# Performance work log

Measured on AMD Instinct MI355X. Metric: run time of the kernel, lower is better.

The kernel has to match this reference:

```python
import jax, jax.numpy as jnp
import numpy as np

FILTER_K = 10      # per-class top-K support retention
TAU = 1.0          # temperature
SCALE = 20.0       # prototype logit scale
EPS = 1e-12


def _normalize(x, axis=-1):
    n = jnp.linalg.norm(x, axis=axis, keepdims=True)
    return x / jnp.maximum(n, EPS)


def _entropy(logits):
    p = jax.nn.softmax(logits, axis=1)
    return -(p * jax.nn.log_softmax(logits, axis=1)).sum(axis=1)


def _quantile(x, q):
    # linear-interpolation quantile (matches torch.quantile default)
    s = jnp.sort(x)
    n = x.shape[0]
    pos = q * (n - 1)
    lo = jnp.floor(pos).astype(jnp.int32)
    hi = jnp.minimum(lo + 1, n - 1)
    frac = pos - lo.astype(x.dtype)
    return s[lo] * (1.0 - frac) + s[hi] * frac


def setup_inputs() -> dict:
    key = jax.random.key(0)
    k1, k2, k3, k4, k5 = jax.random.split(key, 5)
    B, D, C = 65536, 512, 50
    feat = jax.random.normal(k1, (B, D), jnp.float32)
    logits_raw = jax.random.normal(k2, (B, C), jnp.float32)
    logits_aug = jax.random.normal(k3, (B, C), jnp.float32)
    W = jax.random.normal(k4, (C, D), jnp.float32) * 0.05  # classifier weight
    b = jax.random.normal(k5, (C,), jnp.float32) * 0.05    # classifier bias
    return {"feat": feat, "logits_raw": logits_raw, "logits_aug": logits_aug, "W": W, "b": b}


def reference(feat, logits_raw, logits_aug, W, b):
    C, D = W.shape
    # --- warmup memory initialized from classifier weights (as in __init__) ---
    wl = W @ W.T + b                       # (C, C)
    p0 = jax.nn.softmax(wl, axis=1)
    lab0 = jnp.argmax(wl, axis=1)          # (C,)
    ent0 = _entropy(wl)
    conf0 = p0.max(axis=1)

    # --- online batch stats ---
    logits = feat @ W.T + b                # (B, C)
    p = jax.nn.softmax(logits, axis=1)
    yhat = jnp.argmax(logits, axis=1)
    ent = _entropy(logits)
    pmax = p.max(axis=1)

    # dynamic entropy-quantile threshold (ent_thresh=None path)
    m = ent.mean()
    dyn_q = jnp.where(m >= 0.45, 0.25, jnp.where(m >= 0.38, 0.3, 0.4))
    thr = _quantile(ent, dyn_q)
    mask = ent <= thr
    # dual-view consistency gate
    mask &= jnp.argmax(logits_raw, axis=1) == jnp.argmax(logits_aug, axis=1)
    # confidence gate
    conf_thr = jnp.where(m >= 0.45, 0.72, 0.62)
    mask &= pmax >= conf_thr

    # --- grown support memory (warmup + accepted batch samples), static shape + valid mask ---
    supports = jnp.concatenate([W, feat], axis=0)          # (C+B, D)
    lab_idx = jnp.concatenate([lab0, yhat], axis=0)        # (C+B,)
    ents = jnp.concatenate([ent0, ent], axis=0)
    conf = jnp.concatenate([conf0, pmax], axis=0)
    valid = jnp.concatenate([jnp.ones((C,), bool), mask], axis=0)

    # --- per-class top-K lowest-entropy pruning (vectorized over classes) ---
    cls_mask = (lab_idx[None, :] == jnp.arange(C)[:, None]) & valid[None, :]  # (C, C+B)
    masked_ent = jnp.where(cls_mask, ents[None, :], jnp.inf)
    order = jnp.argsort(masked_ent, axis=1)
    ranks = jnp.argsort(order, axis=1)                     # rank of each entry within its class
    keep = (cls_mask & (ranks < FILTER_K)).any(axis=0)     # (C+B,)

    # --- confidence-weighted centroids + cosine-sim classification ---
    S = _normalize(supports)
    onehot = jax.nn.one_hot(lab_idx, C, dtype=supports.dtype)
    lab_w = onehot * jnp.maximum(conf, 1e-6)[:, None] * keep[:, None].astype(supports.dtype)
    denom = jnp.maximum(lab_w.sum(axis=0, keepdims=True), EPS)
    centroids = _normalize((lab_w / denom).T @ S)          # (C, D)
    sim = _normalize(feat) @ centroids.T                   # (B, C)
    return SCALE * sim / max(TAU, 1e-6)
```

## Files before the change

### kernel.cpp

```cpp
#include <hip/hip_runtime.h>
#include <math.h>

constexpr int BN = 65536;
constexpr int DK = 512;
constexpr int CN = 50;
constexpr int FILTK = 10;
constexpr int MB = 128;
constexpr int NKS = DK / 32;
constexpr int SELB = 64;
constexpr int CAP = 6144;

typedef __attribute__((ext_vector_type(8))) short short8;
typedef __attribute__((ext_vector_type(4))) float f4;

constexpr int W_SC     = 0;
constexpr int W_H1     = 64;
constexpr int W_H2LO   = 2112;
constexpr int W_H2HI   = 4160;
constexpr int W_H3LO   = 6208;
constexpr int W_H3HI   = 7232;
constexpr int ZERO_WORDS = 8256;
constexpr int W_WFH    = 8256;
constexpr int W_WFL    = W_WFH + 16384;
constexpr int W_CFH    = W_WFL + 16384;
constexpr int W_CFL    = W_CFH + 16384;
constexpr int W_ENT    = W_CFL + 16384;
constexpr int W_PMAX   = W_ENT  + BN;
constexpr int W_YHAT   = W_PMAX + BN;
constexpr int W_CONS   = W_YHAT + BN;
constexpr int W_NORM   = W_CONS + BN;
constexpr int W_LAB0   = W_NORM + BN;
constexpr int W_ENT0   = W_LAB0 + 64;
constexpr int W_CONF0  = W_ENT0 + 64;
constexpr int W_WNORM  = W_CONF0 + 64;
constexpr int LE_CAP   = BN + 64;
constexpr int W_LECLS  = W_WNORM + 64;
constexpr int W_LEENT  = W_LECLS  + LE_CAP;
constexpr int W_LECONF = W_LEENT  + LE_CAP;
constexpr int W_LEORD  = W_LECONF + LE_CAP;
constexpr int W_LESRC  = W_LEORD  + LE_CAP;

struct Scalars {
    float    sum_ent;
    float    mean;
    float    conf_thr;
    float    frac;
    int      klo;
    int      khi;
    unsigned prefix_lo;
    unsigned rank_lo;
    unsigned prefix_hi;
    unsigned rank_hi;
    float    thr;
    unsigned cnt;
    unsigned done1, done2, done3;
};

__device__ __forceinline__ unsigned fkey(float f) {
    unsigned u = __float_as_uint(f);
    return (u & 0x80000000u) ? ~u : (u | 0x80000000u);
}
__device__ __forceinline__ float funkey(unsigned u) {
    return (u & 0x80000000u) ? __uint_as_float(u & 0x7fffffffu) : __uint_as_float(~u);
}

__device__ __forceinline__ short bf16h(float x) {
    unsigned u = __float_as_uint(x);
    return (short)((u + 0x7fffu + ((u >> 16) & 1u)) >> 16);
}
__device__ __forceinline__ float bf16tof(short h) {
    return __uint_as_float(((unsigned)(unsigned short)h) << 16);
}
__device__ __forceinline__ void cvt8(const float* a, short8& h, short8& l) {
    #pragma unroll
    for (int j = 0; j < 8; j++) {
        short hh = bf16h(a[j]);
        h[j] = hh;
        l[j] = bf16h(a[j] - bf16tof(hh));
    }
}
__device__ __forceinline__ int fragidx(int ks, int n, int q, int j) {
    return ks * 2048 + (n >> 4) * 512 + ((n & 15) + 16 * q) * 8 + j;
}

__global__ void init_kernel(const float* __restrict__ W, const float* __restrict__ bias,
                            int* __restrict__ lab0, float* __restrict__ ent0,
                            float* __restrict__ conf0, float* __restrict__ wnorm,
                            unsigned* __restrict__ wsz,
                            short* __restrict__ wfh, short* __restrict__ wfl) {
    const int b = blockIdx.x, l = threadIdx.x;
    if (b >= 64) {
        for (int i = (b - 64) * 64 + l; i < ZERO_WORDS; i += 128) wsz[i] = 0u;
        return;
    }
    {
        int ks = l >> 2, q = l & 3;
        int dst = fragidx(ks, b, q, 0);
        if (b < CN) {
            const float* wp = W + b * DK + l * 8;
            f4 x = *(const f4*)wp, y = *(const f4*)(wp + 4);
            float a8[8] = {x[0], x[1], x[2], x[3], y[0], y[1], y[2], y[3]};
            short8 h, lo2; cvt8(a8, h, lo2);
            *(short8*)(wfh + dst) = h;
            *(short8*)(wfl + dst) = lo2;
        } else {
            short8 z; 
            #pragma unroll
            for (int j = 0; j < 8; j++) z[j] = 0;
            *(short8*)(wfh + dst) = z;
            *(short8*)(wfl + dst) = z;
        }
    }
    if (b >= CN) return;

    __shared__ float wrow[DK];
    const int i = b;
    f4 v0 = *(const f4*)(W + i * DK + l * 4);
    f4 v1 = *(const f4*)(W + i * DK + 256 + l * 4);
    *(f4*)(wrow + l * 4) = v0;
    *(f4*)(wrow + 256 + l * 4) = v1;
    float sq = v0[0]*v0[0] + v0[1]*v0[1] + v0[2]*v0[2] + v0[3]*v0[3]
             + v1[0]*v1[0] + v1[1]*v1[1] + v1[2]*v1[2] + v1[3]*v1[3];
    #pragma unroll
    for (int m = 1; m < 64; m <<= 1) sq += __shfl_xor(sq, m);
    if (l == 0) wnorm[i] = sqrtf(sq);
    __syncthreads();

    float dot = -INFINITY;
    int   ai  = 0x7fffffff;
    if (l < CN) {
        const float* wj = W + l * DK;
        float d2 = 0.f;
        for (int d = 0; d < DK; d += 4) {
            f4 a = *(const f4*)(wrow + d);
            f4 b4 = *(const f4*)(wj + d);
            d2 = fmaf(a[0], b4[0], fmaf(a[1], b4[1], fmaf(a[2], b4[2], fmaf(a[3], b4[3], d2))));
        }
        dot = d2 + bias[l];
        ai  = l;
    }
    float mx = dot; int am = ai;
    #pragma unroll
    for (int m = 32; m >= 1; m >>= 1) {
        float o = __shfl_xor(mx, m); int oi = __shfl_xor(am, m);
        if (o > mx || (o == mx && oi < am)) { mx = o; am = oi; }
    }
    float e = 0.f, te = 0.f;
    if (l < CN) { e = expf(dot - mx); te = e * (dot - mx); }
    #pragma unroll
    for (int m = 1; m < 64; m <<= 1) { e += __shfl_xor(e, m); te += __shfl_xor(te, m); }
    if (l == 0) {
        lab0[i]  = am;
        ent0[i]  = logf(e) - te / e;
        conf0[i] = 1.f / e;
    }
}

template <int MODE>
__global__ __launch_bounds__(256) void gemm_kernel(
        const float* __restrict__ feat,
        const short* __restrict__ bfh, const short* __restrict__ bfl,
        const float* __restrict__ bias,
        float* __restrict__ ent, float* __restrict__ pmaxA,
        int* __restrict__ yhat, float* __restrict__ rnorm,
        const float* __restrict__ lraw, const float* __restrict__ laug,
        unsigned* __restrict__ consp, Scalars* sc, float* __restrict__ outp) {
    constexpr int LSZ = (MODE == 0) ? MB * 65 : 4;
    __shared__ float L[LSZ];
    const int t = threadIdx.x;
    const int w = t >> 6, lane = t & 63, m = lane & 15, q = lane >> 4;
    const int rb = blockIdx.x * MB + w * 32;

    f4 acc[2][4];
    #pragma unroll
    for (int mt = 0; mt < 2; mt++)
        #pragma unroll
        for (int nt = 0; nt < 4; nt++) acc[mt][nt] = (f4){0.f, 0.f, 0.f, 0.f};
    float sq[2] = {0.f, 0.f};

    for (int ks = 0; ks < NKS; ks++) {
        short8 ah[2], al[2];
        #pragma unroll
        for (int mt = 0; mt < 2; mt++) {
            const float* ap = feat + (size_t)(rb + mt * 16 + m) * DK + ks * 32 + q * 8;
            f4 x = *(const f4*)ap;
            f4 y = *(const f4*)(ap + 4);
            float a8[8] = {x[0], x[1], x[2], x[3], y[0], y[1], y[2], y[3]};
            if (MODE == 0) {
                sq[mt] += x[0]*x[0] + x[1]*x[1] + x[2]*x[2] + x[3]*x[3]
                        + y[0]*y[0] + y[1]*y[1] + y[2]*y[2] + y[3]*y[3];
            }
            cvt8(a8, ah[mt], al[mt]);
        }
        short8 bh[4], bl[4];
        #pragma unroll
        for (int nt = 0; nt < 4; nt++) {
            int off = ks * 2048 + nt * 512 + lane * 8;
            bh[nt] = *(const short8*)(bfh + off);
            bl[nt] = *(const short8*)(bfl + off);
        }
        #pragma unroll
        for (int mt = 0; mt < 2; mt++)
            #pragma unroll
            for (int nt = 0; nt < 4; nt++) {
                acc[mt][nt] = __builtin_amdgcn_mfma_f32_16x16x32_bf16(ah[mt], bh[nt], acc[mt][nt], 0, 0, 0);
                acc[mt][nt] = __builtin_amdgcn_mfma_f32_16x16x32_bf16(al[mt], bh[nt], acc[mt][nt], 0, 0, 0);
                acc[mt][nt] = __builtin_amdgcn_mfma_f32_16x16x32_bf16(ah[mt], bl[nt], acc[mt][nt], 0, 0, 0);
            }
    }

    if (MODE == 0) {
        #pragma unroll
        for (int mt = 0; mt < 2; mt++) {
            float s = sq[mt];
            s += __shfl_xor(s, 16);
            s += __shfl_xor(s, 32);
            if (q == 0) rnorm[rb + mt * 16 + m] = sqrtf(s);
        }
        float bc[4];
        #pragma unroll
        for (int nt = 0; nt < 4; nt++) { int c = nt * 16 + m; bc[nt] = (c < CN) ? bias[c] : 0.f; }
        #pragma unroll
        for (int mt = 0; mt < 2; mt++)
            #pragma unroll
            for (int nt = 0; nt < 4; nt++)
                #pragma unroll
                for (int r = 0; r < 4; r++) {
                    int row = w * 32 + mt * 16 + q * 4 + r;
                    L[row * 65 + nt * 16 + m] = acc[mt][nt][r] + bc[nt];
                }
        __syncthreads();
        if (t < MB) {
            int grow = blockIdx.x * MB + t;
            const float* Lr = L + t * 65;
            float mx = Lr[0]; int am = 0;
            #pragma unroll 10
            for (int j = 1; j < CN; j++) { float v = Lr[j]; if (v > mx) { mx = v; am = j; } }
            float s = 0.f, tt = 0.f;
            for (int j = 0; j < CN; j++) {
                float d = Lr[j] - mx;
                float e = expf(d);
                s += e; tt += e * d;
            }
            float ev = logf(s) - tt / s;
            ent  [grow] = ev;
            pmaxA[grow] = 1.f / s;
            yhat [grow] = am;
            const float* rp  = lraw + (size_t)grow * CN;
            const float* apg = laug + (size_t)grow * CN;
            float m1 = rp[0];  int a1 = 0;
            float m2 = apg[0]; int a2 = 0;
            #pragma unroll 10
            for (int j = 1; j < CN; j++) {
                float v1 = rp[j];  if (v1 > m1) { m1 = v1; a1 = j; }
                float v2 = apg[j]; if (v2 > m2) { m2 = v2; a2 = j; }
            }
            consp[grow] = (a1 == a2) ? 1u : 0u;
            float es = ev;
            #pragma unroll
            for (int mk = 1; mk < 64; mk <<= 1) es += __shfl_xor(es, mk);
            if ((t & 63) == 0) atomicAdd(&sc->sum_ent, es);
        }
    } else {
        #pragma unroll
        for (int mt = 0; mt < 2; mt++)
            #pragma unroll
            for (int r = 0; r < 4; r++) {
                int grow = rb + mt * 16 + q * 4 + r;
                float s = 20.f / fmaxf(rnorm[grow], 1e-12f);
                #pragma unroll
                for (int nt = 0; nt < 4; nt++) {
                    int c = nt * 16 + m;
                    if (c < CN) outp[(size_t)grow * CN + c] = acc[mt][nt][r] * s;
                }
            }
    }
}

__global__ __launch_bounds__(256) void sel1_kernel(const float* __restrict__ ent,
                                                   unsigned* __restrict__ H1, Scalars* sc) {
    __shared__ unsigned h[2048];
    __shared__ unsigned part[256];
    __shared__ int last;
    const int t = threadIdx.x;
    for (int b = t; b < 2048; b += 256) h[b] = 0u;
    __syncthreads();
    const int lo = blockIdx.x * (BN / SELB), hi = lo + (BN / SELB);
    for (int i = lo + t; i < hi; i += 256)
        atomicAdd(&h[fkey(ent[i]) >> 21], 1u);
    __syncthreads();
    for (int b = t; b < 2048; b += 256) if (h[b]) atomicAdd(&H1[b], h[b]);
    __threadfence();
    if (t == 0) last = (atomicAdd(&sc->done1, 1u) == SELB - 1) ? 1 : 0;
    __syncthreads();
    if (!last) return;

    for (int b = t; b < 2048; b += 256) h[b] = atomicAdd(&H1[b], 0u);
    __syncthreads();
    unsigned ps = 0;
    #pragma unroll
    for (int j = 0; j < 8; j++) ps += h[t * 8 + j];
    part[t] = ps;
    __syncthreads();
    if (t == 0) {
        float m = sc->sum_ent / (float)BN;
        sc->mean = m;
        float q = (m >= 0.45f) ? 0.25f : ((m >= 0.38f) ? 0.30f : 0.40f);
        sc->conf_thr = (m >= 0.45f) ? 0.72f : 0.62f;
        float pos = q * (float)(BN - 1);
        float flo = floorf(pos);
        sc->frac = pos - flo;
        int klo = (int)flo;
        int khi = klo + 1; if (khi > BN - 1) khi = BN - 1;
        sc->klo = klo; sc->khi = khi;
        for (int pass = 0; pass < 2; pass++) {
            unsigned k = (pass == 0) ? (unsigned)klo : (unsigned)khi;
            unsigned cum = 0; int c = 0;
            for (; c < 255; c++) { unsigned pc = part[c]; if (cum + pc > k) break; cum += pc; }
            int b = c * 8;
            for (; b < c * 8 + 7; b++) { unsigned hb = h[b]; if (cum + hb > k) break; cum += hb; }
            if (pass == 0) { sc->prefix_lo = (unsigned)b; sc->rank_lo = k - cum; }
            else           { sc->prefix_hi = (unsigned)b; sc->rank_hi = k - cum; }
        }
    }
}

__global__ __launch_bounds__(256) void sel2_kernel(const float* __restrict__ ent,
                                                   unsigned* __restrict__ HLO, unsigned* __restrict__ HHI,
                                                   Scalars* sc) {
    __shared__ unsigned hlo[2048], hhi[2048];
    __shared__ unsigned plo_s[256], phi_s[256];
    __shared__ int last;
    const int t = threadIdx.x;
    const unsigned plo = sc->prefix_lo, phi = sc->prefix_hi;
    for (int b = t; b < 2048; b += 256) { hlo[b] = 0u; hhi[b] = 0u; }
    __syncthreads();
    const int lo = blockIdx.x * (BN / SELB), hi = lo + (BN / SELB);
    for (int i = lo + t; i < hi; i += 256) {
        unsigned u = fkey(ent[i]);
        unsigned d1 = u >> 21, d2 = (u >> 10) & 2047u;
        if (d1 == plo) atomicAdd(&hlo[d2], 1u);
        if (d1 == phi) atomicAdd(&hhi[d2], 1u);
    }
    __syncthreads();
    for (int b = t; b < 2048; b += 256) {
        if (hlo[b]) atomicAdd(&HLO[b], hlo[b]);
        if (hhi[b]) atomicAdd(&HHI[b], hhi[b]);
    }
    __threadfence();
    if (t == 0) last = (atomicAdd(&sc->done2, 1u) == SELB - 1) ? 1 : 0;
    __syncthreads();
    if (!last) return;

    for (int b = t; b < 2048; b += 256) { hlo[b] = atomicAdd(&HLO[b], 0u); hhi[b] = atomicAdd(&HHI[b], 0u); }
    __syncthreads();
    unsigned pl = 0, ph = 0;
    #pragma unroll
    for (int j = 0; j < 8; j++) { pl += hlo[t * 8 + j]; ph += hhi[t * 8 + j]; }
    plo_s[t] = pl; phi_s[t] = ph;
    __syncthreads();
    if (t == 0) {
        {
            unsigned k = sc->rank_lo, cum = 0; int c = 0;
            for (; c < 255; c++) { unsigned pc = plo_s[c]; if (cum + pc > k) break; cum += pc; }
            int b = c * 8;
            for (; b < c * 8 + 7; b++) { unsigned hb = hlo[b]; if (cum + hb > k) break; cum += hb; }
            sc->prefix_lo = (plo << 11) | (unsigned)b; sc->rank_lo = k - cum;
        }
        {
            unsigned k = sc->rank_hi, cum = 0; int c = 0;
            for (; c < 255; c++) { unsigned pc = phi_s[c]; if (cum + pc > k) break; cum += pc; }
            int b = c * 8;
            for (; b < c * 8 + 7; b++) { unsigned hb = hhi[b]; if (cum + hb > k) break; cum += hb; }
            sc->prefix_hi = (phi << 11) | (unsigned)b; sc->rank_hi = k - cum;
        }
    }
}

__global__ __launch_bounds__(256) void sel3_kernel(const float* __restrict__ ent,
                                                   unsigned* __restrict__ HLO, unsigned* __restrict__ HHI,
                                                   Scalars* sc) {
    __shared__ unsigned hlo[1024], hhi[1024];
    __shared__ unsigned plo_s[256], phi_s[256];
    __shared__ int last;
    const int t = threadIdx.x;
    const unsigned plo = sc->prefix_lo, phi = sc->prefix_hi;
    for (int b = t; b < 1024; b += 256) { hlo[b] = 0u; hhi[b] = 0u; }
    __syncthreads();
    const int lo = blockIdx.x * (BN / SELB), hi = lo + (BN / SELB);
    for (int i = lo + t; i < hi; i += 256) {
        unsigned u = fkey(ent[i]);
        unsigned p22 = u >> 10, d3 = u & 1023u;
        if (p22 == plo) atomicAdd(&hlo[d3], 1u);
        if (p22 == phi) atomicAdd(&hhi[d3], 1u);
    }
    __syncthreads();
    for (int b = t; b < 1024; b += 256) {
        if (hlo[b]) atomicAdd(&HLO[b], hlo[b]);
        if (hhi[b]) atomicAdd(&HHI[b], hhi[b]);
    }
    __threadfence();
    if (t == 0) last = (atomicAdd(&sc->done3, 1u) == SELB - 1) ? 1 : 0;
    __syncthreads();
    if (!last) return;

    for (int b = t; b < 1024; b += 256) { hlo[b] = atomicAdd(&HLO[b], 0u); hhi[b] = atomicAdd(&HHI[b], 0u); }
    __syncthreads();
    unsigned pl = 0, ph = 0;
    #pragma unroll
    for (int j = 0; j < 4; j++) { pl += hlo[t * 4 + j]; ph += hhi[t * 4 + j]; }
    plo_s[t] = pl; phi_s[t] = ph;
    __syncthreads();
    if (t == 0) {
        float vlo, vhi;
        {
            unsigned k = sc->rank_lo, cum = 0; int c = 0;
            for (; c < 255; c++) { unsigned pc = plo_s[c]; if (cum + pc > k) break; cum += pc; }
            int b = c * 4;
            for (; b < c * 4 + 3; b++) { unsigned hb = hlo[b]; if (cum + hb > k) break; cum += hb; }
            vlo = funkey((plo << 10) | (unsigned)b);
        }
        {
            unsigned k = sc->rank_hi, cum = 0; int c = 0;
            for (; c < 255; c++) { unsigned pc = phi_s[c]; if (cum + pc > k) break; cum += pc; }
            int b = c * 4;
            for (; b < c * 4 + 3; b++) { unsigned hb = hhi[b]; if (cum + hb > k) break; cum += hb; }
            vhi = funkey((phi << 10) | (unsigned)b);
        }
        sc->thr = vlo * (1.f - sc->frac) + vhi * sc->frac;
    }
}

__global__ __launch_bounds__(256) void compact_kernel(
        const float* __restrict__ ent, const float* __restrict__ pmaxA,
        const int* __restrict__ yhat, const unsigned* __restrict__ cons,
        const int* __restrict__ lab0, const float* __restrict__ ent0,
        const float* __restrict__ conf0, Scalars* sc,
        int* le_cls, float* le_ent, float* le_conf, int* le_ord, int* le_src) {
    int i = blockIdx.x * blockDim.x + threadIdx.x;
    if (i < CN) {
        le_cls[i] = lab0[i]; le_ent[i] = ent0[i]; le_conf[i] = conf0[i];
        le_ord[i] = i; le_src[i] = i;
    }
    if (i >= BN) return;
    bool m = (ent[i] <= sc->thr) && (cons[i] != 0u) && (pmaxA[i] >= sc->conf_thr);
    if (m) {
        int pos = (int)atomicAdd(&sc->cnt, 1u);
        int e = CN + pos;
        le_cls[e] = yhat[i]; le_ent[e] = ent[i]; le_conf[e] = pmaxA[i];
        le_ord[e] = CN + i;  le_src[e] = i;
    }
}

__global__ __launch_bounds__(256) void tail2_kernel(
        const Scalars* sc, const int* __restrict__ le_cls,
        const float* __restrict__ le_ent, const float* __restrict__ le_conf,
        const int* __restrict__ le_ord, const int* __restrict__ le_src,
        const float* __restrict__ W, const float* __restrict__ feat,
        const float* __restrict__ wnorm, const float* __restrict__ rnorm,
        short* __restrict__ cfh, short* __restrict__ cfl) {
    const int c = blockIdx.x, t = threadIdx.x;
    if (c >= CN) {
        for (int idx = t; idx < 512; idx += 256) {
            int ks = idx >> 5, rem = idx & 31, qq = rem >> 3, jj = rem & 7;
            int dst = fragidx(ks, c, qq, jj);
            cfh[dst] = 0; cfl[dst] = 0;
        }
        return;
    }
    __shared__ float sent[CAP];
    __shared__ int   sord[CAP];
    __shared__ float sconf[CAP];
    __shared__ int   ssrc[CAP];
    __shared__ float wk[CAP];
    __shared__ float accv[DK];
    __shared__ float red[4];
    __shared__ int   mc_s;
    if (t == 0) mc_s = 0;
    for (int d = t; d < DK; d += 256) accv[d] = 0.f;
    __syncthreads();
    const int M = CN + (int)sc->cnt;
    for (int e = t; e < M; e += 256) {
        if (le_cls[e] == c) {
            int i = atomicAdd(&mc_s, 1);
            if (i < CAP) { sent[i] = le_ent[e]; sord[i] = le_ord[e]; sconf[i] = le_conf[e]; ssrc[i] = le_src[e]; }
        }
    }
    __syncthreads();
    int mc = min(mc_s, CAP);
    for (int i = t; i < mc; i += 256) {
        float v = sent[i]; int o = sord[i]; int r = 0;
        for (int j = 0; j < mc && r < FILTK; j++)
            if (sent[j] < v || (sent[j] == v && sord[j] < o)) r++;
        wk[i] = (r < FILTK) ? fmaxf(sconf[i], 1e-6f) : 0.f;
    }
    __syncthreads();
    for (int i = 0; i < mc; i++) {
        float wgt = wk[i];
        if (wgt <= 0.f) continue;
        int src = ssrc[i];
        bool warm = sord[i] < CN;
        const float* rowp = warm ? (W + src * DK) : (feat + (size_t)src * DK);
        float nr = warm ? wnorm[src] : rnorm[src];
        float k = wgt / fmaxf(nr, 1e-12f);
        for (int d = t; d < DK; d += 256) accv[d] += k * rowp[d];
    }
    __syncthreads();
    float s = 0.f;
    for (int d = t; d < DK; d += 256) { float v = accv[d]; s = fmaf(v, v, s); }
    #pragma unroll
    for (int mk = 1; mk < 64; mk <<= 1) s += __shfl_xor(s, mk);
    if ((t & 63) == 0) red[t >> 6] = s;
    __syncthreads();
    float inv = 1.f / fmaxf(sqrtf(red[0] + red[1] + red[2] + red[3]), 1e-12f);
    for (int k = t; k < DK; k += 256) {
        float v = accv[k] * inv;
        short hh = bf16h(v);
        short ll = bf16h(v - bf16tof(hh));
        int ks = k >> 5, kk = k & 31, qq = kk >> 3, jj = kk & 7;
        int dst = fragidx(ks, c, qq, jj);
        cfh[dst] = hh; cfl[dst] = ll;
    }
}

extern "C" void kernel_launch(void* const* d_in, const int* in_sizes, int n_in,
                              void* d_out, int out_size, void* d_ws, size_t ws_size,
                              hipStream_t stream) {
    const float* feat = (const float*)d_in[0];
    const float* lraw = (const float*)d_in[1];
    const float* laug = (const float*)d_in[2];
    const float* W    = (const float*)d_in[3];
    const float* bias = (const float*)d_in[4];
    float* out = (float*)d_out;

    unsigned* wsw    = (unsigned*)d_ws;
    Scalars*  sc     = (Scalars*)(wsw + W_SC);
    unsigned* H1     = wsw + W_H1;
    unsigned* H2LO   = wsw + W_H2LO;
    unsigned* H2HI   = wsw + W_H2HI;
    unsigned* H3LO   = wsw + W_H3LO;
    unsigned* H3HI   = wsw + W_H3HI;
    short*    wfh    = (short*)(wsw + W_WFH);
    short*    wfl    = (short*)(wsw + W_WFL);
    short*    cfh    = (short*)(wsw + W_CFH);
    short*    cfl    = (short*)(wsw + W_CFL);
    float*    ent    = (float*)(wsw + W_ENT);
    float*    pmaxA  = (float*)(wsw + W_PMAX);
    int*      yhat   = (int*)(wsw + W_YHAT);
    unsigned* cons   = wsw + W_CONS;
    float*    rnorm  = (float*)(wsw + W_NORM);
    int*      lab0   = (int*)(wsw + W_LAB0);
    float*    ent0   = (float*)(wsw + W_ENT0);
    float*    conf0  = (float*)(wsw + W_CONF0);
    float*    wnorm  = (float*)(wsw + W_WNORM);
    int*      le_cls = (int*)(wsw + W_LECLS);
    float*    le_ent = (float*)(wsw + W_LEENT);
    float*    le_conf= (float*)(wsw + W_LECONF);
    int*      le_ord = (int*)(wsw + W_LEORD);
    int*      le_src = (int*)(wsw + W_LESRC);

    init_kernel<<<66, 64, 0, stream>>>(W, bias, lab0, ent0, conf0, wnorm, wsw, wfh, wfl);
    gemm_kernel<0><<<BN / MB, 256, 0, stream>>>(feat, wfh, wfl, bias, ent, pmaxA, yhat, rnorm,
                                                lraw, laug, cons, sc, nullptr);
    sel1_kernel<<<SELB, 256, 0, stream>>>(ent, H1, sc);
    sel2_kernel<<<SELB, 256, 0, stream>>>(ent, H2LO, H2HI, sc);
    sel3_kernel<<<SELB, 256, 0, stream>>>(ent, H3LO, H3HI, sc);
    compact_kernel<<<BN / 256, 256, 0, stream>>>(ent, pmaxA, yhat, cons, lab0, ent0, conf0, sc,
                                                 le_cls, le_ent, le_conf, le_ord, le_src);
    tail2_kernel<<<64, 256, 0, stream>>>(sc, le_cls, le_ent, le_conf, le_ord, le_src,
                                         W, feat, wnorm, rnorm, cfh, cfl);
    gemm_kernel<1><<<BN / MB, 256, 0, stream>>>(feat, cfh, cfl, nullptr, nullptr, nullptr, nullptr, rnorm,
                                                nullptr, nullptr, nullptr, sc, out);
}
```

Measured before the change: 345.6 us.

## Stage feature tiles through LDS with coalesced loads and halve GEMM block rows

```diff
diff --git a/kernel.cpp b/kernel.cpp
--- a/kernel.cpp
+++ b/kernel.cpp
@@ -5,10 +5,10 @@
 constexpr int DK = 512;
 constexpr int CN = 50;
 constexpr int FILTK = 10;
-constexpr int MB = 128;
-constexpr int NKS = DK / 32;
+constexpr int MB = 64;
 constexpr int SELB = 64;
 constexpr int CAP = 6144;
+constexpr int ASTR = 132;
 
 typedef __attribute__((ext_vector_type(8))) short short8;
 typedef __attribute__((ext_vector_type(4))) float f4;
@@ -104,7 +104,7 @@
             *(short8*)(wfh + dst) = h;
             *(short8*)(wfl + dst) = lo2;
         } else {
-            short8 z; 
+            short8 z;
             #pragma unroll
             for (int j = 0; j < 8; j++) z[j] = 0;
             *(short8*)(wfh + dst) = z;
@@ -165,86 +165,91 @@
         int* __restrict__ yhat, float* __restrict__ rnorm,
         const float* __restrict__ lraw, const float* __restrict__ laug,
         unsigned* __restrict__ consp, Scalars* sc, float* __restrict__ outp) {
-    constexpr int LSZ = (MODE == 0) ? MB * 65 : 4;
-    __shared__ float L[LSZ];
+    __shared__ float As[MB * ASTR];
     const int t = threadIdx.x;
     const int w = t >> 6, lane = t & 63, m = lane & 15, q = lane >> 4;
-    const int rb = blockIdx.x * MB + w * 32;
-
-    f4 acc[2][4];
-    #pragma unroll
-    for (int mt = 0; mt < 2; mt++)
+    const int rb = blockIdx.x * MB;
+    const float* fbase = feat + (size_t)rb * DK;
+
+    f4 acc[4];
+    #pragma unroll
+    for (int nt = 0; nt < 4; nt++) acc[nt] = (f4){0.f, 0.f, 0.f, 0.f};
+    float sq = 0.f;
+
+    const int scol = (t & 31) * 4;
+    const int srow0 = t >> 5;
+
+    for (int kc = 0; kc < 4; kc++) {
+        if (kc) __syncthreads();
         #pragma unroll
-        for (int nt = 0; nt < 4; nt++) acc[mt][nt] = (f4){0.f, 0.f, 0.f, 0.f};
-    float sq[2] = {0.f, 0.f};
-
-    for (int ks = 0; ks < NKS; ks++) {
-        short8 ah[2], al[2];
+        for (int r8 = 0; r8 < 8; r8++) {
+            int row = r8 * 8 + srow0;
+            f4 v = *(const f4*)(fbase + (size_t)row * DK + kc * 128 + scol);
+            *(f4*)(&As[row * ASTR + scol]) = v;
+        }
+        __syncthreads();
         #pragma unroll
-        for (int mt = 0; mt < 2; mt++) {
-            const float* ap = feat + (size_t)(rb + mt * 16 + m) * DK + ks * 32 + q * 8;
+        for (int ks = 0; ks < 4; ks++) {
+            const float* ap = &As[(w * 16 + m) * ASTR + ks * 32 + q * 8];
             f4 x = *(const f4*)ap;
             f4 y = *(const f4*)(ap + 4);
             float a8[8] = {x[0], x[1], x[2], x[3], y[0], y[1], y[2], y[3]};
             if (MODE == 0) {
-                sq[mt] += x[0]*x[0] + x[1]*x[1] + x[2]*x[2] + x[3]*x[3]
-                        + y[0]*y[0] + y[1]*y[1] + y[2]*y[2] + y[3]*y[3];
-            }
-            cvt8(a8, ah[mt], al[mt]);
-        }
-        short8 bh[4], bl[4];
-        #pragma unroll
-        for (int nt = 0; nt < 4; nt++) {
-            int off = ks * 2048 + nt * 512 + lane * 8;
-            bh[nt] = *(const short8*)(bfh + off);
-            bl[nt] = *(const short8*)(bfl + off);
-        }
-        #pragma unroll
-        for (int mt = 0; mt < 2; mt++)
+                sq += x[0]*x[0] + x[1]*x[1] + x[2]*x[2] + x[3]*x[3]
+                    + y[0]*y[0] + y[1]*y[1] + y[2]*y[2] + y[3]*y[3];
+            }
+            short8 ah, al;
+            cvt8(a8, ah, al);
+            const int ksg = kc * 4 + ks;
+            short8 bh[4], bl[4];
             #pragma unroll
             for (int nt = 0; nt < 4; nt++) {
-                acc[mt][nt] = __builtin_amdgcn_mfma_f32_16x16x32_bf16(ah[mt], bh[nt], acc[mt][nt], 0, 0, 0);
-                acc[mt][nt] = __builtin_amdgcn_mfma_f32_16x16x32_bf16(al[mt], bh[nt], acc[mt][nt], 0, 0, 0);
-                acc[mt][nt] = __builtin_amdgcn_mfma_f32_16x16x32_bf16(ah[mt], bl[nt], acc[mt][nt], 0, 0, 0);
-            }
+                int off = ksg * 2048 + nt * 512 + lane * 8;
+                bh[nt] = *(const short8*)(bfh + off);
+                bl[nt] = *(const short8*)(bfl + off);
+            }
+            #pragma unroll
+            for (int nt = 0; nt < 4; nt++) {
+                acc[nt] = __builtin_amdgcn_mfma_f32_16x16x32_bf16(ah, bh[nt], acc[nt], 0, 0, 0);
+                acc[nt] = __builtin_amdgcn_mfma_f32_16x16x32_bf16(al, bh[nt], acc[nt], 0, 0, 0);
+                acc[nt] = __builtin_amdgcn_mfma_f32_16x16x32_bf16(ah, bl[nt], acc[nt], 0, 0, 0);
+            }
+        }
     }
 
     if (MODE == 0) {
-        #pragma unroll
-        for (int mt = 0; mt < 2; mt++) {
-            float s = sq[mt];
-            s += __shfl_xor(s, 16);
-            s += __shfl_xor(s, 32);
-            if (q == 0) rnorm[rb + mt * 16 + m] = sqrtf(s);
-        }
+        float s = sq;
+        s += __shfl_xor(s, 16);
+        s += __shfl_xor(s, 32);
+        if (q == 0) rnorm[rb + w * 16 + m] = sqrtf(s);
+        __syncthreads();
+        float* L = As;
         float bc[4];
         #pragma unroll
         for (int nt = 0; nt < 4; nt++) { int c = nt * 16 + m; bc[nt] = (c < CN) ? bias[c] : 0.f; }
         #pragma unroll
-        for (int mt = 0; mt < 2; mt++)
+        for (int nt = 0; nt < 4; nt++)
             #pragma unroll
-            for (int nt = 0; nt < 4; nt++)
-                #pragma unroll
-                for (int r = 0; r < 4; r++) {
-                    int row = w * 32 + mt * 16 + q * 4 + r;
-                    L[row * 65 + nt * 16 + m] = acc[mt][nt][r] + bc[nt];
-                }
+            for (int r = 0; r < 4; r++) {
+                int row = w * 16 + q * 4 + r;
+                L[row * 65 + nt * 16 + m] = acc[nt][r] + bc[nt];
+            }
         __syncthreads();
         if (t < MB) {
-            int grow = blockIdx.x * MB + t;
+            int grow = rb + t;
             const float* Lr = L + t * 65;
             float mx = Lr[0]; int am = 0;
             #pragma unroll 10
             for (int j = 1; j < CN; j++) { float v = Lr[j]; if (v > mx) { mx = v; am = j; } }
-            float s = 0.f, tt = 0.f;
+            float ssum = 0.f, tt = 0.f;
             for (int j = 0; j < CN; j++) {
                 float d = Lr[j] - mx;
                 float e = expf(d);
-                s += e; tt += e * d;
-            }
-            float ev = logf(s) - tt / s;
+                ssum += e; tt += e * d;
+            }
+            float ev = logf(ssum) - tt / ssum;
             ent  [grow] = ev;
-            pmaxA[grow] = 1.f / s;
+            pmaxA[grow] = 1.f / ssum;
             yhat [grow] = am;
             const float* rp  = lraw + (size_t)grow * CN;
             const float* apg = laug + (size_t)grow * CN;
@@ -259,21 +264,19 @@
             float es = ev;
             #pragma unroll
             for (int mk = 1; mk < 64; mk <<= 1) es += __shfl_xor(es, mk);
-            if ((t & 63) == 0) atomicAdd(&sc->sum_ent, es);
+            if (t == 0) atomicAdd(&sc->sum_ent, es);
         }
     } else {
         #pragma unroll
-        for (int mt = 0; mt < 2; mt++)
+        for (int r = 0; r < 4; r++) {
+            int grow = rb + w * 16 + q * 4 + r;
+            float s = 20.f / fmaxf(rnorm[grow], 1e-12f);
             #pragma unroll
-            for (int r = 0; r < 4; r++) {
-                int grow = rb + mt * 16 + q * 4 + r;
-                float s = 20.f / fmaxf(rnorm[grow], 1e-12f);
-                #pragma unroll
-                for (int nt = 0; nt < 4; nt++) {
-                    int c = nt * 16 + m;
-                    if (c < CN) outp[(size_t)grow * CN + c] = acc[mt][nt][r] * s;
-                }
-            }
+            for (int nt = 0; nt < 4; nt++) {
+                int c = nt * 16 + m;
+                if (c < CN) outp[(size_t)grow * CN + c] = acc[nt][r] * s;
+            }
+        }
     }
 }
 
```

New measurement: 357.5 us. +3.5%, slower.
